# Performance work log

Measured on AMD Instinct MI355X. Metric: run time of the kernel, lower is better.

Reference implementation:

```python
import jax, jax.numpy as jnp
import numpy as np

N_NODES = 50000
N_EDGES = 800000
F_IN = 128
HID = 128
F_OUT = 2


def setup_inputs() -> dict:
    key = jax.random.key(0)
    ks = jax.random.split(key, 12)
    s = lambda d: 1.0 / np.sqrt(d)
    return {
        "x": jax.random.normal(ks[0], (N_NODES, F_IN), dtype=jnp.float32),
        "edge_index": jax.random.randint(ks[1], (2, N_EDGES), 0, N_NODES, dtype=jnp.int64),
        "W1_root": jax.random.normal(ks[2], (F_IN, HID), dtype=jnp.float32) * s(F_IN),
        "W1_nbr": jax.random.normal(ks[3], (F_IN, HID), dtype=jnp.float32) * s(F_IN),
        "b1": jnp.zeros((HID,), dtype=jnp.float32),
        "W2_root": jax.random.normal(ks[4], (HID, HID), dtype=jnp.float32) * s(HID),
        "W2_nbr": jax.random.normal(ks[5], (HID, HID), dtype=jnp.float32) * s(HID),
        "b2": jnp.zeros((HID,), dtype=jnp.float32),
        "Wa": jax.random.normal(ks[6], (HID, HID), dtype=jnp.float32) * s(HID),
        "a_src": jax.random.normal(ks[7], (HID,), dtype=jnp.float32) * s(HID),
        "a_dst": jax.random.normal(ks[8], (HID,), dtype=jnp.float32) * s(HID),
        "Wfc": jax.random.normal(ks[9], (HID, F_OUT), dtype=jnp.float32) * s(HID),
        "bfc": jnp.zeros((F_OUT,), dtype=jnp.float32),
    }


def reference(x, edge_index, W1_root, W1_nbr, b1, W2_root, W2_nbr, b2,
              Wa, a_src, a_dst, Wfc, bfc):
    src = edge_index[0]
    dst = edge_index[1]
    N = x.shape[0]

    def graph_conv(h, Wr, Wn, b):
        # sum-aggregate neighbor features, then two linear maps (PyG GraphConv)
        agg = jax.ops.segment_sum(h[src], dst, num_segments=N)  # [N, d]
        return h @ Wr + agg @ Wn + b

    h = jax.nn.relu(graph_conv(x, W1_root, W1_nbr, b1))
    h = jax.nn.relu(graph_conv(h, W2_root, W2_nbr, b2))

    # GAT-style attention: e_ij = LeakyReLU(a_src . Wh_j + a_dst . Wh_i)
    ht = h @ Wa                      # [N, HID]
    s_src = ht @ a_src               # [N]
    s_dst = ht @ a_dst               # [N]
    e = jax.nn.leaky_relu(s_src[src] + s_dst[dst], negative_slope=0.2)  # [E]

    # segment softmax over incoming edges of each destination node
    m = jax.ops.segment_max(e, dst, num_segments=N)          # [N]
    ee = jnp.exp(e - m[dst])                                  # [E]
    denom = jax.ops.segment_sum(ee, dst, num_segments=N)     # [N]
    alpha = ee / (denom[dst] + 1e-16)                         # [E]

    out = jax.ops.segment_sum(alpha[:, None] * ht[src], dst, num_segments=N)  # [N, HID]
    return out @ Wfc + bfc
```

## Files before the change

### kernel.cpp

```cpp
#include <hip/hip_runtime.h>
#include <cstddef>
#include <cstdint>


typedef __attribute__((ext_vector_type(8))) short short8;
typedef __attribute__((ext_vector_type(4))) float f32x4;

#define NBUK 128
#define BSH  9
#define CHUNK 1568

__device__ __forceinline__ ushort f2b(float f) {
  uint32_t u = __float_as_uint(f);
  u += 0x7fffu + ((u >> 16) & 1u);
  return (ushort)(u >> 16);
}
__device__ __forceinline__ float b2f(ushort h) {
  return __uint_as_float(((uint32_t)h) << 16);
}

__device__ __forceinline__ void gload_lds16(const void* g, void* l) {
  __builtin_amdgcn_global_load_lds(
      (const __attribute__((address_space(1))) void*)g,
      (__attribute__((address_space(3))) void*)l, 16, 0, 0);
}


__global__ __launch_bounds__(256) void split_kernel(
    const float* __restrict__ in, ushort* __restrict__ hi,
    ushort* __restrict__ lo, int n) {
  int i = (blockIdx.x * blockDim.x + threadIdx.x) * 8;
  if (i >= n) return;
  float4 v0 = *(const float4*)(in + i);
  float4 v1 = *(const float4*)(in + i + 4);
  float v[8] = {v0.x, v0.y, v0.z, v0.w, v1.x, v1.y, v1.z, v1.w};
  short8 h, l;
  #pragma unroll
  for (int b = 0; b < 8; ++b) {
    ushort hh = f2b(v[b]);
    h[b] = (short)hh;
    l[b] = (short)f2b(v[b] - b2f(hh));
  }
  *(short8*)(hi + i) = h;
  *(short8*)(lo + i) = l;
}


__global__ __launch_bounds__(256) void wsplit_kernel(
    const float* __restrict__ W0, const float* __restrict__ W1,
    const float* __restrict__ W2, const float* __restrict__ W3,
    const float* __restrict__ W4,
    ushort* __restrict__ WhT, ushort* __restrict__ WlT) {
  __shared__ float tile[128][128];
  int m = blockIdx.x;
  const float* W = (m == 0) ? W0 : (m == 1) ? W1 : (m == 2) ? W2 : (m == 3) ? W3 : W4;
  int t = threadIdx.x;
  #pragma unroll
  for (int i = 0; i < 64; ++i) {
    int idx = i * 256 + t;
    tile[idx >> 7][idx & 127] = W[idx];
  }
  __syncthreads();
  int j = t >> 1, k0 = (t & 1) * 64;
  size_t obase = (size_t)m * 16384 + (size_t)j * 128 + k0;
  #pragma unroll
  for (int c = 0; c < 8; ++c) {
    short8 h, l;
    #pragma unroll
    for (int b = 0; b < 8; ++b) {
      float v = tile[k0 + c * 8 + b][j];
      ushort hh = f2b(v);
      h[b] = (short)hh;
      l[b] = (short)f2b(v - b2f(hh));
    }
    *(short8*)(WhT + obase + c * 8) = h;
    *(short8*)(WlT + obase + c * 8) = l;
  }
}


__global__ __launch_bounds__(256) void bhist_kernel(
    const int* __restrict__ ei, int E, int* __restrict__ bcnt) {
  __shared__ int lh[NBUK];
  int t = threadIdx.x;
  if (t < NBUK) lh[t] = 0;
  __syncthreads();
  int base = blockIdx.x * CHUNK;
  int lim = base + CHUNK; if (lim > E) lim = E;
  for (int i = base + t; i < lim; i += 256) atomicAdd(&lh[ei[E + i] >> BSH], 1);
  __syncthreads();
  if (t < NBUK && lh[t]) atomicAdd(&bcnt[t], lh[t]);
}

__global__ __launch_bounds__(256) void bscan_kernel(
    const int* __restrict__ bcnt, int* __restrict__ bbase,
    int* __restrict__ gtail) {
  __shared__ int sA[NBUK], sB[NBUK];
  int t = threadIdx.x;
  if (t < NBUK) sA[t] = bcnt[t];
  __syncthreads();
  int *s = sA, *d = sB;
  for (int st = 1; st < NBUK; st <<= 1) {
    if (t < NBUK) d[t] = s[t] + ((t >= st) ? s[t - st] : 0);
    __syncthreads();
    int* tmp = s; s = d; d = tmp;
  }
  if (t < NBUK) {
    int exc = (t == 0) ? 0 : s[t - 1];
    bbase[t] = exc;
    gtail[t] = exc;
  }
  if (t == 0) bbase[NBUK] = s[NBUK - 1];
}

__global__ __launch_bounds__(256) void bscatter_kernel(
    const int* __restrict__ ei, int E, int* __restrict__ gtail,
    uint2* __restrict__ pair) {
  __shared__ int lh[NBUK], sB[NBUK], lofs[NBUK], lcur[NBUK], gbase[NBUK];
  __shared__ uint2 buf[CHUNK];
  int t = threadIdx.x;
  if (t < NBUK) lh[t] = 0;
  __syncthreads();
  int base = blockIdx.x * CHUNK;
  int lim = base + CHUNK; if (lim > E) lim = E;
  for (int i = base + t; i < lim; i += 256) atomicAdd(&lh[ei[E + i] >> BSH], 1);
  __syncthreads();
  int *s = lh, *d = sB;
  for (int st = 1; st < NBUK; st <<= 1) {
    if (t < NBUK) d[t] = s[t] + ((t >= st) ? s[t - st] : 0);
    __syncthreads();
    int* tmp = s; s = d; d = tmp;
  }
  if (t < NBUK) {
    lofs[t] = (t == 0) ? 0 : s[t - 1];
    lcur[t] = lofs[t];
  }
  __syncthreads();
  for (int i = base + t; i < lim; i += 256) {
    int srcv = ei[i], dstv = ei[E + i];
    int p = atomicAdd(&lcur[dstv >> BSH], 1);
    buf[p] = make_uint2((unsigned)srcv, (unsigned)dstv);
  }
  __syncthreads();
  if (t < NBUK) {
    int c = s[t] - lofs[t];
    gbase[t] = c ? atomicAdd(&gtail[t], c) : 0;
  }
  __syncthreads();
  int n = lim - base;
  for (int i = t; i < n; i += 256) {
    uint2 pr = buf[i];
    int b = ((int)pr.y) >> BSH;
    pair[gbase[b] + (i - lofs[b])] = pr;
  }
}

__global__ __launch_bounds__(256) void csrbuild_kernel(
    const uint2* __restrict__ pair, const int* __restrict__ bbase,
    int* __restrict__ ofs, int* __restrict__ csr, int N, int E) {
  __shared__ int hA[512], hB[512];
  int b = blockIdx.x, t = threadIdx.x;
  int base = bbase[b], cnt = bbase[b + 1] - base;
  int node0 = b << BSH;
  int nn = N - node0; if (nn > 512) nn = 512;
  hA[t] = 0; hA[t + 256] = 0;
  __syncthreads();
  for (int i = t; i < cnt; i += 256)
    atomicAdd(&hA[(int)pair[base + i].y - node0], 1);
  __syncthreads();
  int *s = hA, *d = hB;
  for (int st = 1; st < 512; st <<= 1) {
    #pragma unroll
    for (int k = 0; k < 2; ++k) {
      int i = t + k * 256;
      d[i] = s[i] + ((i >= st) ? s[i - st] : 0);
    }
    __syncthreads();
    int* tmp = s; s = d; d = tmp;
  }
  #pragma unroll
  for (int k = 0; k < 2; ++k) {
    int i = t + k * 256;
    if (i < nn) ofs[node0 + i] = base + (i == 0 ? 0 : s[i - 1]);
  }
  if (t == 0 && node0 + nn >= N) ofs[N] = E;
  #pragma unroll
  for (int k = 0; k < 2; ++k) {
    int i = t + k * 256;
    d[i] = (i == 0 ? 0 : s[i - 1]);
  }
  __syncthreads();
  for (int i = t; i < cnt; i += 256) {
    uint2 pr = pair[base + i];
    int p = atomicAdd(&d[(int)pr.y - node0], 1);
    csr[base + p] = (int)pr.x;
  }
}


__global__ __launch_bounds__(256) void agg_kernel(
    const ushort* __restrict__ Xh, const int* __restrict__ csr,
    const int* __restrict__ ofs, ushort* __restrict__ Gh,
    ushort* __restrict__ Gl, int N) {
  int node = (blockIdx.x * blockDim.x + threadIdx.x) >> 6;
  int lane = threadIdx.x & 63;
  if (node >= N) return;
  int g = lane >> 4, q = lane & 15;
  int beg = ofs[node], end = ofs[node + 1];
  float a[8] = {};
  int p = beg + g;
  if (p < end) {
    int s = csr[p];
    short8 v = *(const short8*)(Xh + (size_t)s * 128 + q * 8);
    for (p += 4; p < end; p += 4) {
      int s2 = csr[p];
      short8 v2 = *(const short8*)(Xh + (size_t)s2 * 128 + q * 8);
      #pragma unroll
      for (int b = 0; b < 8; ++b) a[b] += b2f((ushort)v[b]);
      v = v2;
    }
    #pragma unroll
    for (int b = 0; b < 8; ++b) a[b] += b2f((ushort)v[b]);
  }
  #pragma unroll
  for (int b = 0; b < 8; ++b) {
    a[b] += __shfl_xor(a[b], 16);
    a[b] += __shfl_xor(a[b], 32);
  }
  if (lane < 16) {
    short8 h, l;
    #pragma unroll
    for (int b = 0; b < 8; ++b) {
      ushort hh = f2b(a[b]);
      h[b] = (short)hh;
      l[b] = (short)f2b(a[b] - b2f(hh));
    }
    *(short8*)(Gh + (size_t)node * 128 + q * 8) = h;
    *(short8*)(Gl + (size_t)node * 128 + q * 8) = l;
  }
}


template <int S, bool RELU, bool BIAS>
__global__ __launch_bounds__(512, 2) void mgemm_kernel(
    const ushort* __restrict__ A1h, const ushort* __restrict__ A1l,
    const ushort* __restrict__ A2h, const ushort* __restrict__ A2l,
    const ushort* __restrict__ WhT, const ushort* __restrict__ WlT,
    const float* __restrict__ bias,
    ushort* __restrict__ Ch, ushort* __restrict__ Cl, int M) {
  __shared__ char lds[2 * S * 16384];
  int t = threadIdx.x;
  int l = t & 63;
  int w = t >> 6;
  int j = (w << 4) + (l & 15);
  int krow0 = (l >> 4) * 8;
  int rowBase = blockIdx.x * 64;

  const ushort* srcs[4] = {A1h, A1l, (S > 1) ? A2h : A1h, (S > 1) ? A2l : A1l};
  int ldsWaveBase0 = (t & ~63) * 16;
  #pragma unroll
  for (int q = 0; q < 2 * S; ++q) {
    const char* gsrc = (const char*)srcs[q];
    #pragma unroll
    for (int part = 0; part < 2; ++part) {
      int c = part * 512 + t;
      int r = c >> 4;
      int cb = (c & 15) << 4;
      int row = rowBase + r;
      if (row >= M) row = M - 1;
      int sb = cb ^ ((r & 7) << 4);
      gload_lds16(gsrc + (size_t)row * 256 + sb,
                  &lds[q * 16384 + part * 8192 + ldsWaveBase0]);
    }
  }

  short8 wh[S][4], wl[S][4];
  #pragma unroll
  for (int s = 0; s < S; ++s) {
    #pragma unroll
    for (int ks = 0; ks < 4; ++ks) {
      size_t wb = (size_t)s * 16384 + (size_t)j * 128 + ks * 32 + krow0;
      wh[s][ks] = *(const short8*)(WhT + wb);
      wl[s][ks] = *(const short8*)(WlT + wb);
    }
  }

  __syncthreads();

  f32x4 acc[4];
  #pragma unroll
  for (int i = 0; i < 4; ++i) acc[i] = (f32x4){0.f, 0.f, 0.f, 0.f};

  #pragma unroll
  for (int rf = 0; rf < 4; ++rf) {
    int r = rf * 16 + (l & 15);
    int sw = (r & 7) << 4;
    int rb = r * 256;
    #pragma unroll
    for (int s = 0; s < S; ++s) {
      #pragma unroll
      for (int ks = 0; ks < 4; ++ks) {
        int off = rb + ((ks * 64 + (l >> 4) * 16) ^ sw);
        short8 ah = *(const short8*)&lds[(s * 2 + 0) * 16384 + off];
        short8 al = *(const short8*)&lds[(s * 2 + 1) * 16384 + off];
        acc[rf] = __builtin_amdgcn_mfma_f32_16x16x32_bf16(al, wh[s][ks], acc[rf], 0, 0, 0);
        acc[rf] = __builtin_amdgcn_mfma_f32_16x16x32_bf16(ah, wl[s][ks], acc[rf], 0, 0, 0);
        acc[rf] = __builtin_amdgcn_mfma_f32_16x16x32_bf16(ah, wh[s][ks], acc[rf], 0, 0, 0);
      }
    }
  }

  float bj = BIAS ? bias[j] : 0.f;
  #pragma unroll
  for (int rf = 0; rf < 4; ++rf) {
    int rbase = rowBase + rf * 16 + (l >> 4) * 4;
    #pragma unroll
    for (int r = 0; r < 4; ++r) {
      int row = rbase + r;
      if (row < M) {
        float v = acc[rf][r];
        if (BIAS) v += bj;
        if (RELU) v = fmaxf(v, 0.f);
        ushort h = f2b(v);
        Ch[(size_t)row * 128 + j] = h;
        Cl[(size_t)row * 128 + j] = f2b(v - b2f(h));
      }
    }
  }
}


__global__ __launch_bounds__(256) void dots_kernel(
    const ushort* __restrict__ HTh, const ushort* __restrict__ HTl,
    const float* __restrict__ a_src, const float* __restrict__ a_dst,
    float* __restrict__ ssrc, float* __restrict__ sdst, int N) {
  int n = (blockIdx.x * blockDim.x + threadIdx.x) >> 6;
  int lane = threadIdx.x & 63;
  if (n >= N) return;
  uint uh = ((const uint*)(HTh + (size_t)n * 128))[lane];
  uint ul = ((const uint*)(HTl + (size_t)n * 128))[lane];
  float h0 = b2f((ushort)(uh & 0xffff)) + b2f((ushort)(ul & 0xffff));
  float h1 = b2f((ushort)(uh >> 16)) + b2f((ushort)(ul >> 16));
  float vs = h0 * a_src[2 * lane] + h1 * a_src[2 * lane + 1];
  float vd = h0 * a_dst[2 * lane] + h1 * a_dst[2 * lane + 1];
  #pragma unroll
  for (int d = 32; d > 0; d >>= 1) {
    vs += __shfl_xor(vs, d);
    vd += __shfl_xor(vd, d);
  }
  if (lane == 0) { ssrc[n] = vs; sdst[n] = vd; }
}


__global__ __launch_bounds__(256) void attn_kernel(
    const ushort* __restrict__ HTh, const int* __restrict__ csr,
    const int* __restrict__ ofs, const float* __restrict__ ssrc,
    const float* __restrict__ sdst, const float* __restrict__ Wfc,
    const float* __restrict__ bfc, float* __restrict__ out, int N) {
  __shared__ float eld[4][128];
  int wv = (threadIdx.x >> 6) & 3;
  int n = (blockIdx.x * blockDim.x + threadIdx.x) >> 6;
  int lane = threadIdx.x & 63;
  if (n >= N) return;
  int beg = ofs[n], end = ofs[n + 1];
  int deg = end - beg;
  float sd = sdst[n];

  float m = -3.4e38f;
  for (int i = lane; i < deg; i += 64) {
    float e = ssrc[csr[beg + i]] + sd;
    e = (e >= 0.f) ? e : 0.2f * e;
    if (i < 128) eld[wv][i] = e;
    m = fmaxf(m, e);
  }
  #pragma unroll
  for (int d = 32; d > 0; d >>= 1) m = fmaxf(m, __shfl_xor(m, d));

  float ssum = 0.f;
  for (int i = lane; i < deg; i += 64) {
    float e;
    if (i < 128) e = eld[wv][i];
    else {
      e = ssrc[csr[beg + i]] + sd;
      e = (e >= 0.f) ? e : 0.2f * e;
    }
    float t = __expf(e - m);
    if (i < 128) eld[wv][i] = t;
    ssum += t;
  }
  #pragma unroll
  for (int d = 32; d > 0; d >>= 1) ssum += __shfl_xor(ssum, d);
  float inv = 1.0f / (ssum + 1e-16f);

  int g = lane >> 4, q = lane & 15;
  float a[8] = {};
  int i = g;
  if (i < deg) {
    int s = csr[beg + i];
    short8 v = *(const short8*)(HTh + (size_t)s * 128 + q * 8);
    float t;
    if (i < 128) t = eld[wv][i];
    else {
      float e = ssrc[s] + sd;
      e = (e >= 0.f) ? e : 0.2f * e;
      t = __expf(e - m);
    }
    for (i += 4; i < deg; i += 4) {
      int s2 = csr[beg + i];
      short8 v2 = *(const short8*)(HTh + (size_t)s2 * 128 + q * 8);
      float t2;
      if (i < 128) t2 = eld[wv][i];
      else {
        float e2 = ssrc[s2] + sd;
        e2 = (e2 >= 0.f) ? e2 : 0.2f * e2;
        t2 = __expf(e2 - m);
      }
      float wgt = t * inv;
      #pragma unroll
      for (int b = 0; b < 8; ++b) a[b] += wgt * b2f((ushort)v[b]);
      v = v2; t = t2;
    }
    float wgt = t * inv;
    #pragma unroll
    for (int b = 0; b < 8; ++b) a[b] += wgt * b2f((ushort)v[b]);
  }
  #pragma unroll
  for (int b = 0; b < 8; ++b) {
    a[b] += __shfl_xor(a[b], 16);
    a[b] += __shfl_xor(a[b], 32);
  }

  float4 wf0 = *(const float4*)(Wfc + q * 16);
  float4 wf1 = *(const float4*)(Wfc + q * 16 + 4);
  float4 wf2 = *(const float4*)(Wfc + q * 16 + 8);
  float4 wf3 = *(const float4*)(Wfc + q * 16 + 12);
  float o0 = a[0] * wf0.x + a[1] * wf0.z + a[2] * wf1.x + a[3] * wf1.z +
             a[4] * wf2.x + a[5] * wf2.z + a[6] * wf3.x + a[7] * wf3.z;
  float o1 = a[0] * wf0.y + a[1] * wf0.w + a[2] * wf1.y + a[3] * wf1.w +
             a[4] * wf2.y + a[5] * wf2.w + a[6] * wf3.y + a[7] * wf3.w;
  #pragma unroll
  for (int d = 1; d < 16; d <<= 1) {
    o0 += __shfl_xor(o0, d);
    o1 += __shfl_xor(o1, d);
  }
  if (lane == 0) {
    out[(size_t)n * 2 + 0] = o0 + bfc[0];
    out[(size_t)n * 2 + 1] = o1 + bfc[1];
  }
}


static inline size_t align_up(size_t x, size_t a) { return (x + a - 1) & ~(a - 1); }

extern "C" void kernel_launch(void* const* d_in, const int* in_sizes, int n_in,
                              void* d_out, int out_size, void* d_ws, size_t ws_size,
                              hipStream_t stream) {
  const float* x     = (const float*)d_in[0];
  const int*   ei    = (const int*)d_in[1];
  const float* W1r   = (const float*)d_in[2];
  const float* W1n   = (const float*)d_in[3];
  const float* b1    = (const float*)d_in[4];
  const float* W2r   = (const float*)d_in[5];
  const float* W2n   = (const float*)d_in[6];
  const float* b2    = (const float*)d_in[7];
  const float* Wa    = (const float*)d_in[8];
  const float* a_src = (const float*)d_in[9];
  const float* a_dst = (const float*)d_in[10];
  const float* Wfc   = (const float*)d_in[11];
  const float* bfc   = (const float*)d_in[12];

  const int N = in_sizes[0] / 128;
  const int E = in_sizes[1] / 2;

  char* ws = (char*)d_ws;
  size_t off = 0;
  auto take = [&](size_t bytes) {
    char* p = ws + off;
    off = align_up(off + bytes, 256);
    return p;
  };
  const size_t NB = (size_t)N * 128 * 2;
  int*    ofs   = (int*)take((size_t)(N + 1) * 4);
  int*    csr   = (int*)take((size_t)E * 4);
  int*    bcnt  = (int*)take(NBUK * 4);
  int*    bbase = (int*)take((NBUK + 1) * 4);
  int*    gtail = (int*)take(NBUK * 4);
  uint2*  pair  = (uint2*)take((size_t)E * 8);
  float*  ssrc  = (float*)take((size_t)N * 4);
  float*  sdst  = (float*)take((size_t)N * 4);
  ushort* whT   = (ushort*)take((size_t)5 * 16384 * 2);
  ushort* wlT   = (ushort*)take((size_t)5 * 16384 * 2);
  ushort* bA    = (ushort*)take(NB);
  ushort* bB    = (ushort*)take(NB);
  ushort* bC    = (ushort*)take(NB);
  ushort* bD    = (ushort*)take(NB);
  ushort* bE    = (ushort*)take(NB);
  ushort* bF    = (ushort*)take(NB);

  hipMemsetAsync(bcnt, 0, NBUK * 4, stream);

  const int nodeBlocks = (N + 3) / 4;
  const int gemmBlocks = (N + 63) / 64;
  const int splitBlocks = (N * 128 / 8 + 255) / 256;
  const int chunkBlocks = (E + CHUNK - 1) / CHUNK;
  const int bukBlocks   = (N + 511) / 512;

  wsplit_kernel<<<5, 256, 0, stream>>>(W1r, W1n, W2r, W2n, Wa, whT, wlT);
  split_kernel<<<splitBlocks, 256, 0, stream>>>(x, bA, bB, N * 128);
  bhist_kernel<<<chunkBlocks, 256, 0, stream>>>(ei, E, bcnt);
  bscan_kernel<<<1, 256, 0, stream>>>(bcnt, bbase, gtail);
  bscatter_kernel<<<chunkBlocks, 256, 0, stream>>>(ei, E, gtail, pair);
  csrbuild_kernel<<<bukBlocks, 256, 0, stream>>>(pair, bbase, ofs, csr, N, E);

  agg_kernel<<<nodeBlocks, 256, 0, stream>>>(bA, csr, ofs, bC, bD, N);
  mgemm_kernel<2, true, true><<<gemmBlocks, 512, 0, stream>>>(
      bA, bB, bC, bD, whT, wlT, b1, bE, bF, N);

  agg_kernel<<<nodeBlocks, 256, 0, stream>>>(bE, csr, ofs, bC, bD, N);
  mgemm_kernel<2, true, true><<<gemmBlocks, 512, 0, stream>>>(
      bE, bF, bC, bD, whT + 2 * 16384, wlT + 2 * 16384, b2, bA, bB, N);

  mgemm_kernel<1, false, false><<<gemmBlocks, 512, 0, stream>>>(
      bA, bB, nullptr, nullptr, whT + 4 * 16384, wlT + 4 * 16384,
      nullptr, bC, bD, N);
  dots_kernel<<<nodeBlocks, 256, 0, stream>>>(bC, bD, a_src, a_dst, ssrc, sdst, N);

  attn_kernel<<<nodeBlocks, 256, 0, stream>>>(
      bC, csr, ofs, ssrc, sdst, Wfc, bfc, (float*)d_out, N);
}
```

Measured before the change: 263.4 us.

## Fuse attention score dots into final GEMM epilogue and deepen gather pipelining

Removes the separate dots_kernel by computing s_src/s_dst inside the last GEMM's epilogue, using shuffle reductions plus an LDS cross-wave reduction, so the HT buffers are not reread. The gather loops in agg and attn now prefetch two rows ahead instead of one and unpack bf16 pairs with cheaper bit ops. The attention kernel applies the softmax normalization once after the reduction instead of per edge. The fused dots use fp32 accumulators rather than the rounded hi+lo values, and the extra LDS and registers could lower GEMM occupancy.

Result: no change. 260.4 us (-1.2%).

```diff
diff --git a/kernel.cpp b/kernel.cpp
--- a/kernel.cpp
+++ b/kernel.cpp
@@ -18,12 +18,26 @@
 __device__ __forceinline__ float b2f(ushort h) {
   return __uint_as_float(((uint32_t)h) << 16);
 }
+__device__ __forceinline__ float blo(uint32_t u) { return __uint_as_float(u << 16); }
+__device__ __forceinline__ float bhi(uint32_t u) { return __uint_as_float(u & 0xffff0000u); }
 
 __device__ __forceinline__ void gload_lds16(const void* g, void* l) {
   __builtin_amdgcn_global_load_lds(
       (const __attribute__((address_space(1))) void*)g,
       (__attribute__((address_space(3))) void*)l, 16, 0, 0);
 }
+
+#define ACC8(A, V)                                     \
+  { A[0] += blo(V.x); A[1] += bhi(V.x);                \
+    A[2] += blo(V.y); A[3] += bhi(V.y);                \
+    A[4] += blo(V.z); A[5] += bhi(V.z);                \
+    A[6] += blo(V.w); A[7] += bhi(V.w); }
+
+#define ACC8W(A, V, T)                                 \
+  { A[0] += (T) * blo(V.x); A[1] += (T) * bhi(V.x);    \
+    A[2] += (T) * blo(V.y); A[3] += (T) * bhi(V.y);    \
+    A[4] += (T) * blo(V.z); A[5] += (T) * bhi(V.z);    \
+    A[6] += (T) * blo(V.w); A[7] += (T) * bhi(V.w); }
 
 
 __global__ __launch_bounds__(256) void split_kernel(
@@ -210,17 +224,19 @@
   float a[8] = {};
   int p = beg + g;
   if (p < end) {
-    int s = csr[p];
-    short8 v = *(const short8*)(Xh + (size_t)s * 128 + q * 8);
-    for (p += 4; p < end; p += 4) {
-      int s2 = csr[p];
-      short8 v2 = *(const short8*)(Xh + (size_t)s2 * 128 + q * 8);
-      #pragma unroll
-      for (int b = 0; b < 8; ++b) a[b] += b2f((ushort)v[b]);
-      v = v2;
-    }
-    #pragma unroll
-    for (int b = 0; b < 8; ++b) a[b] += b2f((ushort)v[b]);
+    uint4 v0 = *(const uint4*)(Xh + (size_t)csr[p] * 128 + q * 8);
+    int p1 = p + 4;
+    if (p1 < end) {
+      uint4 v1 = *(const uint4*)(Xh + (size_t)csr[p1] * 128 + q * 8);
+      for (int pn = p1 + 4; pn < end; pn += 4) {
+        uint4 v2 = *(const uint4*)(Xh + (size_t)csr[pn] * 128 + q * 8);
+        ACC8(a, v0);
+        v0 = v1; v1 = v2;
+      }
+      ACC8(a, v0);
+      v0 = v1;
+    }
+    ACC8(a, v0);
   }
   #pragma unroll
   for (int b = 0; b < 8; ++b) {
@@ -241,14 +257,17 @@
 }
 
 
-template <int S, bool RELU, bool BIAS>
+template <int S, bool RELU, bool BIAS, bool DOTS>
 __global__ __launch_bounds__(512, 2) void mgemm_kernel(
     const ushort* __restrict__ A1h, const ushort* __restrict__ A1l,
     const ushort* __restrict__ A2h, const ushort* __restrict__ A2l,
     const ushort* __restrict__ WhT, const ushort* __restrict__ WlT,
     const float* __restrict__ bias,
+    const float* __restrict__ asp, const float* __restrict__ adp,
+    float* __restrict__ ssrc, float* __restrict__ sdst,
     ushort* __restrict__ Ch, ushort* __restrict__ Cl, int M) {
   __shared__ char lds[2 * S * 16384];
+  __shared__ float pm[DOTS ? 8 * 128 : 1];
   int t = threadIdx.x;
   int l = t & 63;
   int w = t >> 6;
@@ -327,28 +346,42 @@
       }
     }
   }
-}
-
-
-__global__ __launch_bounds__(256) void dots_kernel(
-    const ushort* __restrict__ HTh, const ushort* __restrict__ HTl,
-    const float* __restrict__ a_src, const float* __restrict__ a_dst,
-    float* __restrict__ ssrc, float* __restrict__ sdst, int N) {
-  int n = (blockIdx.x * blockDim.x + threadIdx.x) >> 6;
-  int lane = threadIdx.x & 63;
-  if (n >= N) return;
-  uint uh = ((const uint*)(HTh + (size_t)n * 128))[lane];
-  uint ul = ((const uint*)(HTl + (size_t)n * 128))[lane];
-  float h0 = b2f((ushort)(uh & 0xffff)) + b2f((ushort)(ul & 0xffff));
-  float h1 = b2f((ushort)(uh >> 16)) + b2f((ushort)(ul >> 16));
-  float vs = h0 * a_src[2 * lane] + h1 * a_src[2 * lane + 1];
-  float vd = h0 * a_dst[2 * lane] + h1 * a_dst[2 * lane + 1];
-  #pragma unroll
-  for (int d = 32; d > 0; d >>= 1) {
-    vs += __shfl_xor(vs, d);
-    vd += __shfl_xor(vd, d);
-  }
-  if (lane == 0) { ssrc[n] = vs; sdst[n] = vd; }
+
+  if constexpr (DOTS) {
+    float as_ = asp[j], ad_ = adp[j];
+    #pragma unroll
+    for (int rf = 0; rf < 4; ++rf) {
+      #pragma unroll
+      for (int r = 0; r < 4; ++r) {
+        float v = acc[rf][r];
+        float vs = v * as_, vd = v * ad_;
+        #pragma unroll
+        for (int d = 1; d < 16; d <<= 1) {
+          vs += __shfl_xor(vs, d);
+          vd += __shfl_xor(vd, d);
+        }
+        if ((l & 15) == 0) {
+          int rl = rf * 16 + (l >> 4) * 4 + r;
+          pm[w * 128 + rl * 2 + 0] = vs;
+          pm[w * 128 + rl * 2 + 1] = vd;
+        }
+      }
+    }
+    __syncthreads();
+    if (t < 64) {
+      int row = rowBase + t;
+      if (row < M) {
+        float vs = 0.f, vd = 0.f;
+        #pragma unroll
+        for (int ww = 0; ww < 8; ++ww) {
+          vs += pm[ww * 128 + t * 2 + 0];
+          vd += pm[ww * 128 + t * 2 + 1];
+        }
+        ssrc[row] = vs;
+        sdst[row] = vd;
+      }
+    }
+  }
 }
 
 
@@ -394,40 +427,51 @@
 
   int g = lane >> 4, q = lane & 15;
   float a[8] = {};
-  int i = g;
-  if (i < deg) {
-    int s = csr[beg + i];
-    short8 v = *(const short8*)(HTh + (size_t)s * 128 + q * 8);
-    float t;
-    if (i < 128) t = eld[wv][i];
+  int i0 = g;
+  if (i0 < deg) {
+    int s0 = csr[beg + i0];
+    uint4 v0 = *(const uint4*)(HTh + (size_t)s0 * 128 + q * 8);
+    float t0;
+    if (i0 < 128) t0 = eld[wv][i0];
     else {
-      float e = ssrc[s] + sd;
+      float e = ssrc[s0] + sd;
       e = (e >= 0.f) ? e : 0.2f * e;
-      t = __expf(e - m);
-    }
-    for (i += 4; i < deg; i += 4) {
-      int s2 = csr[beg + i];
-      short8 v2 = *(const short8*)(HTh + (size_t)s2 * 128 + q * 8);
-      float t2;
-      if (i < 128) t2 = eld[wv][i];
+      t0 = __expf(e - m);
+    }
+    int i1 = i0 + 4;
+    if (i1 < deg) {
+      int s1 = csr[beg + i1];
+      uint4 v1 = *(const uint4*)(HTh + (size_t)s1 * 128 + q * 8);
+      float t1;
+      if (i1 < 128) t1 = eld[wv][i1];
       else {
-        float e2 = ssrc[s2] + sd;
-        e2 = (e2 >= 0.f) ? e2 : 0.2f * e2;
-        t2 = __expf(e2 - m);
-      }
-      float wgt = t * inv;
-      #pragma unroll
-      for (int b = 0; b < 8; ++b) a[b] += wgt * b2f((ushort)v[b]);
-      v = v2; t = t2;
-    }
-    float wgt = t * inv;
-    #pragma unroll
-    for (int b = 0; b < 8; ++b) a[b] += wgt * b2f((ushort)v[b]);
+        float e = ssrc[s1] + sd;
+        e = (e >= 0.f) ? e : 0.2f * e;
+        t1 = __expf(e - m);
+      }
+      for (int i2 = i1 + 4; i2 < deg; i2 += 4) {
+        int s2 = csr[beg + i2];
+        uint4 v2 = *(const uint4*)(HTh + (size_t)s2 * 128 + q * 8);
+        float t2;
+        if (i2 < 128) t2 = eld[wv][i2];
+        else {
+          float e = ssrc[s2] + sd;
+          e = (e >= 0.f) ? e : 0.2f * e;
+          t2 = __expf(e - m);
+        }
+        ACC8W(a, v0, t0);
+        v0 = v1; t0 = t1; v1 = v2; t1 = t2;
+      }
+      ACC8W(a, v0, t0);
+      v0 = v1; t0 = t1;
+    }
+    ACC8W(a, v0, t0);
   }
   #pragma unroll
   for (int b = 0; b < 8; ++b) {
     a[b] += __shfl_xor(a[b], 16);
     a[b] += __shfl_xor(a[b], 32);
+    a[b] *= inv;
   }
 
   float4 wf0 = *(const float4*)(Wfc + q * 16);
@@ -513,17 +557,18 @@
   csrbuild_kernel<<<bukBlocks, 256, 0, stream>>>(pair, bbase, ofs, csr, N, E);
 
   agg_kernel<<<nodeBlocks, 256, 0, stream>>>(bA, csr, ofs, bC, bD, N);
-  mgemm_kernel<2, true, true><<<gemmBlocks, 512, 0, stream>>>(
-      bA, bB, bC, bD, whT, wlT, b1, bE, bF, N);
+  mgemm_kernel<2, true, true, false><<<gemmBlocks, 512, 0, stream>>>(
+      bA, bB, bC, bD, whT, wlT, b1, nullptr, nullptr, nullptr, nullptr,
+      bE, bF, N);
 
   agg_kernel<<<nodeBlocks, 256, 0, stream>>>(bE, csr, ofs, bC, bD, N);
-  mgemm_kernel<2, true, true><<<gemmBlocks, 512, 0, stream>>>(
-      bE, bF, bC, bD, whT + 2 * 16384, wlT + 2 * 16384, b2, bA, bB, N);
-
-  mgemm_kernel<1, false, false><<<gemmBlocks, 512, 0, stream>>>(
-      bA, bB, nullptr, nullptr, whT + 4 * 16384, wlT + 4 * 16384,
-      nullptr, bC, bD, N);
-  dots_kernel<<<nodeBlocks, 256, 0, stream>>>(bC, bD, a_src, a_dst, ssrc, sdst, N);
+  mgemm_kernel<2, true, true, false><<<gemmBlocks, 512, 0, stream>>>(
+      bE, bF, bC, bD, whT + 2 * 16384, wlT + 2 * 16384, b2, nullptr, nullptr,
+      nullptr, nullptr, bA, bB, N);
+
+  mgemm_kernel<1, false, false, true><<<gemmBlocks, 512, 0, stream>>>(
+      bA, bB, nullptr, nullptr, whT + 4 * 16384, wlT + 4 * 16384, nullptr,
+      a_src, a_dst, ssrc, sdst, bC, bD, N);
 
   attn_kernel<<<nodeBlocks, 256, 0, stream>>>(
       bC, csr, ofs, ssrc, sdst, Wfc, bfc, (float*)d_out, N);
```
